# Optimization experiments

Measured on AMD Instinct MI355X. Metric: run time of the kernel, lower is better.

The kernel has to match this reference:

```python
import jax, jax.numpy as jnp
import numpy as np

L, E, D, R, B = 3, 4, 1024, 64, 32768

def setup_inputs() -> dict:
    key = jax.random.key(0)
    ks = jax.random.split(key, 6)
    sU = (2.0 / (D + R)) ** 0.5  # xavier_normal std for [E, D, R]
    sC = (2.0 / (R + R)) ** 0.5
    sG = (2.0 / (D + 1)) ** 0.5
    return {
        "inputs": jax.random.normal(ks[0], (B, D), jnp.float32),
        "U": jax.random.normal(ks[1], (L, E, D, R), jnp.float32) * sU,
        "V": jax.random.normal(ks[2], (L, E, D, R), jnp.float32) * sU,
        "C": jax.random.normal(ks[3], (L, E, R, R), jnp.float32) * sC,
        "gating_w": jax.random.normal(ks[4], (E, D), jnp.float32) * sG,
        "bias": jnp.zeros((L, D), jnp.float32),
    }

def reference(inputs, U, V, C, gating_w, bias):
    x0 = inputs            # [B, D]
    x_l = inputs           # [B, D]
    for i in range(L):
        # per-expert gating scores on current x_l, softmax over experts
        gate = jax.nn.softmax(jnp.einsum("bd,ed->be", x_l, gating_w), axis=1)  # [B, E]
        # low-rank cross: V^T x -> tanh -> C v -> tanh -> U v
        v = jnp.tanh(jnp.einsum("bd,edr->ber", x_l, V[i]))     # [B, E, R]
        v = jnp.tanh(jnp.einsum("ers,bes->ber", C[i], v))      # [B, E, R]
        uv = jnp.einsum("edr,ber->bed", U[i], v)               # [B, E, D]
        dot = x0[:, None, :] * (uv + bias[i][None, None, :])   # [B, E, D]
        moe = jnp.einsum("bed,be->bd", dot, gate)              # [B, D]
        x_l = moe + x_l
    return x_l
```

## Files before the change

kernel.cpp:

```cpp
#include <hip/hip_runtime.h>
#include <hip/hip_bf16.h>

typedef __bf16 bf16_t;
typedef bf16_t bf16x8 __attribute__((ext_vector_type(8)));
typedef float f32x4 __attribute__((ext_vector_type(4)));

#define L_NUM 3
#define E_NUM 4
#define D_DIM 1024
#define R_DIM 64
#define B_ROWS 32768
#define BT 32
#define TPB 512
#define N1 272
#define XL_STRIDE 1032
#define T1_STRIDE 264

#define VT_ELEMS (L_NUM * N1 * D_DIM)
#define UT_ELEMS (L_NUM * D_DIM * 256)
#define CB_ELEMS (L_NUM * E_NUM * R_DIM * R_DIM)

#define MFMA16(a, b, c) __builtin_amdgcn_mfma_f32_16x16x32_bf16((a), (b), (c), 0, 0, 0)

__device__ __forceinline__ ushort f2b(float f) {
  union { float f; unsigned u; } x; x.f = f;
  unsigned r = (x.u + 0x7fffu + ((x.u >> 16) & 1u)) >> 16;
  return (ushort)r;
}
__device__ __forceinline__ float b2f(ushort h) {
  union { unsigned u; float f; } x; x.u = ((unsigned)h) << 16;
  return x.f;
}
__device__ __forceinline__ float tanh_fast(float x) {
  float cx = fminf(fmaxf(x, -15.f), 15.f);
  float e = __expf(2.f * cx);
  return (e - 1.f) / (e + 1.f);
}


__global__ void pack_vt_kernel(const float* __restrict__ V, const float* __restrict__ gw,
                               ushort* __restrict__ vt) {
  int idx = blockIdx.x * 256 + threadIdx.x;
  if (idx >= VT_ELEMS) return;
  int d = idx & (D_DIM - 1);
  int n = (idx >> 10) % N1;
  int l = idx / (N1 * D_DIM);
  float val = 0.f;
  if (n < 256) {
    int e = n >> 6, r = n & 63;
    val = V[(((l * E_NUM + e) * D_DIM) + d) * R_DIM + r];
  } else if (n < 260) {
    val = gw[(n - 256) * D_DIM + d];
  }
  vt[idx] = f2b(val);
}

__global__ void pack_ut_kernel(const float* __restrict__ U, ushort* __restrict__ ut) {
  int idx = blockIdx.x * 256 + threadIdx.x;
  if (idx >= UT_ELEMS) return;
  int er = idx & 255;
  int d = (idx >> 8) & (D_DIM - 1);
  int l = idx >> 18;
  int e = er >> 6, r = er & 63;
  ut[idx] = f2b(U[((l * E_NUM + e) * D_DIM + d) * R_DIM + r]);
}

__global__ void pack_cb_kernel(const float* __restrict__ C, ushort* __restrict__ cb) {
  int idx = blockIdx.x * 256 + threadIdx.x;
  if (idx >= CB_ELEMS) return;
  cb[idx] = f2b(C[idx]);
}


__global__ __launch_bounds__(TPB, 2) void crossnet_fused(
    const float* __restrict__ inputs, const float* __restrict__ bias,
    const ushort* __restrict__ Vt, const ushort* __restrict__ Ut,
    const ushort* __restrict__ Cb, float* __restrict__ out) {
  __shared__ ushort xl[BT * XL_STRIDE];
  __shared__ ushort x0s[BT * XL_STRIDE];
  __shared__ ushort t1[BT * T1_STRIDE];
  __shared__ float glog[BT * 4];
  __shared__ float gate[BT * 4];

  const int tid = threadIdx.x;
  const int wave = tid >> 6;
  const int lane = tid & 63;
  const int l15 = lane & 15;
  const int quad = lane >> 4;
  const long rowbase = (long)blockIdx.x * BT;

  #pragma unroll
  for (int i = 0; i < 16; ++i) {
    int idx = tid + i * TPB;
    int r = idx >> 8;
    int c4 = idx & 255;
    float4 v = ((const float4*)(inputs + (rowbase + r) * D_DIM))[c4];
    ushort4 h;
    h.x = f2b(v.x); h.y = f2b(v.y); h.z = f2b(v.z); h.w = f2b(v.w);
    *(ushort4*)&xl[r * XL_STRIDE + c4 * 4] = h;
    *(ushort4*)&x0s[r * XL_STRIDE + c4 * 4] = h;
  }

  float xlr[8][2][4];
  #pragma unroll
  for (int nt = 0; nt < 8; ++nt)
    #pragma unroll
    for (int m = 0; m < 2; ++m)
      #pragma unroll
      for (int rg = 0; rg < 4; ++rg) {
        int row = m * 16 + quad * 4 + rg;
        int col = wave * 128 + nt * 16 + l15;
        xlr[nt][m][rg] = inputs[(rowbase + row) * D_DIM + col];
      }
  __syncthreads();

  const f32x4 zf = {0.f, 0.f, 0.f, 0.f};

  for (int l = 0; l < L_NUM; ++l) {
    const ushort* vtl = Vt + l * N1 * D_DIM;
    const ushort* utl = Ut + l * D_DIM * 256;
    const ushort* cbl = Cb + l * E_NUM * R_DIM * R_DIM;

    f32x4 acc1[3][2];
    #pragma unroll
    for (int t = 0; t < 3; ++t) { acc1[t][0] = zf; acc1[t][1] = zf; }

    const ushort* xa0 = &xl[l15 * XL_STRIDE + quad * 8];
    const ushort* xa1 = &xl[(16 + l15) * XL_STRIDE + quad * 8];
    const ushort* vb0 = vtl + (wave * 32 + l15) * D_DIM + quad * 8;
    const ushort* vb1 = vb0 + 16 * D_DIM;
    if (wave == 7) {
      const ushort* vb2 = vtl + (256 + l15) * D_DIM + quad * 8;
      #pragma unroll 4
      for (int k0 = 0; k0 < D_DIM; k0 += 32) {
        bf16x8 a0 = *(const bf16x8*)(xa0 + k0);
        bf16x8 a1 = *(const bf16x8*)(xa1 + k0);
        bf16x8 b0 = *(const bf16x8*)(vb0 + k0);
        bf16x8 b1 = *(const bf16x8*)(vb1 + k0);
        bf16x8 b2 = *(const bf16x8*)(vb2 + k0);
        acc1[0][0] = MFMA16(a0, b0, acc1[0][0]);
        acc1[0][1] = MFMA16(a1, b0, acc1[0][1]);
        acc1[1][0] = MFMA16(a0, b1, acc1[1][0]);
        acc1[1][1] = MFMA16(a1, b1, acc1[1][1]);
        acc1[2][0] = MFMA16(a0, b2, acc1[2][0]);
        acc1[2][1] = MFMA16(a1, b2, acc1[2][1]);
      }
    } else {
      #pragma unroll 4
      for (int k0 = 0; k0 < D_DIM; k0 += 32) {
        bf16x8 a0 = *(const bf16x8*)(xa0 + k0);
        bf16x8 a1 = *(const bf16x8*)(xa1 + k0);
        bf16x8 b0 = *(const bf16x8*)(vb0 + k0);
        bf16x8 b1 = *(const bf16x8*)(vb1 + k0);
        acc1[0][0] = MFMA16(a0, b0, acc1[0][0]);
        acc1[0][1] = MFMA16(a1, b0, acc1[0][1]);
        acc1[1][0] = MFMA16(a0, b1, acc1[1][0]);
        acc1[1][1] = MFMA16(a1, b1, acc1[1][1]);
      }
    }

    #pragma unroll
    for (int t = 0; t < 2; ++t) {
      int ncol = wave * 32 + t * 16 + l15;
      #pragma unroll
      for (int m = 0; m < 2; ++m)
        #pragma unroll
        for (int rg = 0; rg < 4; ++rg) {
          int row = m * 16 + quad * 4 + rg;
          t1[row * T1_STRIDE + ncol] = f2b(tanh_fast(acc1[t][m][rg]));
        }
    }
    if (wave == 7 && l15 < 4) {
      #pragma unroll
      for (int m = 0; m < 2; ++m)
        #pragma unroll
        for (int rg = 0; rg < 4; ++rg)
          glog[(m * 16 + quad * 4 + rg) * 4 + l15] = acc1[2][m][rg];
    }
    __syncthreads();

    if (tid < BT) {
      float g0 = glog[tid * 4 + 0], g1 = glog[tid * 4 + 1];
      float g2 = glog[tid * 4 + 2], g3 = glog[tid * 4 + 3];
      float mx = fmaxf(fmaxf(g0, g1), fmaxf(g2, g3));
      float e0 = __expf(g0 - mx), e1 = __expf(g1 - mx);
      float e2 = __expf(g2 - mx), e3 = __expf(g3 - mx);
      float inv = 1.f / (e0 + e1 + e2 + e3);
      gate[tid * 4 + 0] = e0 * inv; gate[tid * 4 + 1] = e1 * inv;
      gate[tid * 4 + 2] = e2 * inv; gate[tid * 4 + 3] = e3 * inv;
    }

    const int e = wave >> 1;
    const int nh = wave & 1;
    f32x4 acc2[2][2];
    acc2[0][0] = zf; acc2[0][1] = zf; acc2[1][0] = zf; acc2[1][1] = zf;
    #pragma unroll
    for (int k0 = 0; k0 < 64; k0 += 32) {
      bf16x8 a0 = *(const bf16x8*)&t1[l15 * T1_STRIDE + e * 64 + k0 + quad * 8];
      bf16x8 a1 = *(const bf16x8*)&t1[(16 + l15) * T1_STRIDE + e * 64 + k0 + quad * 8];
      bf16x8 b0 = *(const bf16x8*)&cbl[(e * 64 + nh * 32 + l15) * 64 + k0 + quad * 8];
      bf16x8 b1 = *(const bf16x8*)&cbl[(e * 64 + nh * 32 + 16 + l15) * 64 + k0 + quad * 8];
      acc2[0][0] = MFMA16(a0, b0, acc2[0][0]);
      acc2[0][1] = MFMA16(a1, b0, acc2[0][1]);
      acc2[1][0] = MFMA16(a0, b1, acc2[1][0]);
      acc2[1][1] = MFMA16(a1, b1, acc2[1][1]);
    }
    __syncthreads();
    #pragma unroll
    for (int t = 0; t < 2; ++t) {
      int ncol = e * 64 + nh * 32 + t * 16 + l15;
      #pragma unroll
      for (int m = 0; m < 2; ++m)
        #pragma unroll
        for (int rg = 0; rg < 4; ++rg) {
          int row = m * 16 + quad * 4 + rg;
          float g = gate[row * 4 + e];
          t1[row * T1_STRIDE + ncol] = f2b(g * tanh_fast(acc2[t][m][rg]));
        }
    }
    __syncthreads();

    f32x4 acc3[8][2];
    #pragma unroll
    for (int nt = 0; nt < 8; ++nt) { acc3[nt][0] = zf; acc3[nt][1] = zf; }
    const ushort* wa0 = &t1[l15 * T1_STRIDE + quad * 8];
    const ushort* wa1 = &t1[(16 + l15) * T1_STRIDE + quad * 8];
    const ushort* ub = utl + (wave * 128 + l15) * 256 + quad * 8;
    #pragma unroll 2
    for (int k0 = 0; k0 < 256; k0 += 32) {
      bf16x8 a0 = *(const bf16x8*)(wa0 + k0);
      bf16x8 a1 = *(const bf16x8*)(wa1 + k0);
      #pragma unroll
      for (int nt = 0; nt < 8; ++nt) {
        bf16x8 b = *(const bf16x8*)(ub + nt * 16 * 256 + k0);
        acc3[nt][0] = MFMA16(a0, b, acc3[nt][0]);
        acc3[nt][1] = MFMA16(a1, b, acc3[nt][1]);
      }
    }

    #pragma unroll
    for (int nt = 0; nt < 8; ++nt) {
      int col = wave * 128 + nt * 16 + l15;
      float bv = bias[l * D_DIM + col];
      #pragma unroll
      for (int m = 0; m < 2; ++m)
        #pragma unroll
        for (int rg = 0; rg < 4; ++rg) {
          int row = m * 16 + quad * 4 + rg;
          float x0v = b2f(x0s[row * XL_STRIDE + col]);
          float xn = xlr[nt][m][rg] + x0v * (acc3[nt][m][rg] + bv);
          xlr[nt][m][rg] = xn;
          xl[row * XL_STRIDE + col] = f2b(xn);
        }
    }
    __syncthreads();
  }

  #pragma unroll
  for (int nt = 0; nt < 8; ++nt) {
    int col = wave * 128 + nt * 16 + l15;
    #pragma unroll
    for (int m = 0; m < 2; ++m)
      #pragma unroll
      for (int rg = 0; rg < 4; ++rg) {
        int row = m * 16 + quad * 4 + rg;
        out[(rowbase + row) * D_DIM + col] = xlr[nt][m][rg];
      }
  }
}

extern "C" void kernel_launch(void* const* d_in, const int* in_sizes, int n_in,
                              void* d_out, int out_size, void* d_ws, size_t ws_size,
                              hipStream_t stream) {
  (void)in_sizes; (void)n_in; (void)out_size; (void)ws_size;
  const float* inputs = (const float*)d_in[0];
  const float* U      = (const float*)d_in[1];
  const float* V      = (const float*)d_in[2];
  const float* C      = (const float*)d_in[3];
  const float* gw     = (const float*)d_in[4];
  const float* bias   = (const float*)d_in[5];
  float* out = (float*)d_out;

  ushort* vt = (ushort*)d_ws;
  ushort* ut = vt + VT_ELEMS;
  ushort* cb = ut + UT_ELEMS;

  pack_vt_kernel<<<(VT_ELEMS + 255) / 256, 256, 0, stream>>>(V, gw, vt);
  pack_ut_kernel<<<(UT_ELEMS + 255) / 256, 256, 0, stream>>>(U, ut);
  pack_cb_kernel<<<(CB_ELEMS + 255) / 256, 256, 0, stream>>>(C, cb);

  crossnet_fused<<<B_ROWS / BT, TPB, 0, stream>>>(inputs, bias, vt, ut, cb, out);
}
```

Before: 685.0 us.

## Shrink LDS and registers with swizzled bf16 residual and in-register x0

Drops the padded fp32 residual held in registers and the separate x0 shared buffer. The residual now lives only as bf16 in an XOR-swizzled shared tile, and x0 is kept as packed bf16 pairs in registers. Gating softmax is computed with wave shuffles and passed through a global workspace. The U projection is split into two halves, the final layer writes the output directly, and launch bounds ask for 4 blocks per CU. The aim is to cut LDS and register use so more blocks fit per CU, and to avoid bank conflicts without padding. The risks are register spills under the tighter bound and extra rounding from carrying the residual in bf16 between layers.

```diff
diff --git a/kernel.cpp b/kernel.cpp
--- a/kernel.cpp
+++ b/kernel.cpp
@@ -8,17 +8,15 @@
 #define L_NUM 3
 #define E_NUM 4
 #define D_DIM 1024
-#define R_DIM 64
 #define B_ROWS 32768
 #define BT 32
 #define TPB 512
 #define N1 272
-#define XL_STRIDE 1032
-#define T1_STRIDE 264
 
 #define VT_ELEMS (L_NUM * N1 * D_DIM)
 #define UT_ELEMS (L_NUM * D_DIM * 256)
-#define CB_ELEMS (L_NUM * E_NUM * R_DIM * R_DIM)
+#define CB_ELEMS (L_NUM * E_NUM * 64 * 64)
+#define GWS_BYTE_OFF ((VT_ELEMS + UT_ELEMS + CB_ELEMS) * 2)
 
 #define MFMA16(a, b, c) __builtin_amdgcn_mfma_f32_16x16x32_bf16((a), (b), (c), 0, 0, 0)
 
@@ -31,10 +29,19 @@
   union { unsigned u; float f; } x; x.u = ((unsigned)h) << 16;
   return x.f;
 }
+__device__ __forceinline__ float u2f_lo(unsigned u) {
+  union { unsigned u; float f; } x; x.u = u << 16; return x.f;
+}
+__device__ __forceinline__ float u2f_hi(unsigned u) {
+  union { unsigned u; float f; } x; x.u = u & 0xffff0000u; return x.f;
+}
 __device__ __forceinline__ float tanh_fast(float x) {
   float cx = fminf(fmaxf(x, -15.f), 15.f);
   float e = __expf(2.f * cx);
   return (e - 1.f) / (e + 1.f);
+}
+__device__ __forceinline__ int swz(int r, int c, int cols) {
+  return r * cols + ((((c >> 3) ^ (r & 7)) << 3) | (c & 7));
 }
 
 
@@ -48,7 +55,7 @@
   float val = 0.f;
   if (n < 256) {
     int e = n >> 6, r = n & 63;
-    val = V[(((l * E_NUM + e) * D_DIM) + d) * R_DIM + r];
+    val = V[(((l * E_NUM + e) * D_DIM) + d) * 64 + r];
   } else if (n < 260) {
     val = gw[(n - 256) * D_DIM + d];
   }
@@ -62,7 +69,7 @@
   int d = (idx >> 8) & (D_DIM - 1);
   int l = idx >> 18;
   int e = er >> 6, r = er & 63;
-  ut[idx] = f2b(U[((l * E_NUM + e) * D_DIM + d) * R_DIM + r]);
+  ut[idx] = f2b(U[((l * E_NUM + e) * D_DIM + d) * 64 + r]);
 }
 
 __global__ void pack_cb_kernel(const float* __restrict__ C, ushort* __restrict__ cb) {
@@ -72,22 +79,22 @@
 }
 
 
-__global__ __launch_bounds__(TPB, 2) void crossnet_fused(
+__global__ __launch_bounds__(TPB, 4) void crossnet_fused(
     const float* __restrict__ inputs, const float* __restrict__ bias,
     const ushort* __restrict__ Vt, const ushort* __restrict__ Ut,
-    const ushort* __restrict__ Cb, float* __restrict__ out) {
-  __shared__ ushort xl[BT * XL_STRIDE];
-  __shared__ ushort x0s[BT * XL_STRIDE];
-  __shared__ ushort t1[BT * T1_STRIDE];
-  __shared__ float glog[BT * 4];
-  __shared__ float gate[BT * 4];
+    const ushort* __restrict__ Cb, float* __restrict__ gws,
+    float* __restrict__ out) {
+  __shared__ ushort xl[BT * 1024];
+  __shared__ ushort t1s[BT * 256];
 
   const int tid = threadIdx.x;
   const int wave = tid >> 6;
   const int lane = tid & 63;
   const int l15 = lane & 15;
   const int quad = lane >> 4;
+  const int r7 = l15 & 7;
   const long rowbase = (long)blockIdx.x * BT;
+  float* gwb = gws + (long)blockIdx.x * (BT * E_NUM);
 
   #pragma unroll
   for (int i = 0; i < 16; ++i) {
@@ -97,47 +104,50 @@
     float4 v = ((const float4*)(inputs + (rowbase + r) * D_DIM))[c4];
     ushort4 h;
     h.x = f2b(v.x); h.y = f2b(v.y); h.z = f2b(v.z); h.w = f2b(v.w);
-    *(ushort4*)&xl[r * XL_STRIDE + c4 * 4] = h;
-    *(ushort4*)&x0s[r * XL_STRIDE + c4 * 4] = h;
+    int off = r * 1024 + ((((c4 >> 1) ^ (r & 7)) << 3) | ((c4 & 1) << 2));
+    *(ushort4*)&xl[off] = h;
   }
-
-  float xlr[8][2][4];
+  __syncthreads();
+
+  unsigned x0p[8][2][2];
   #pragma unroll
-  for (int nt = 0; nt < 8; ++nt)
+  for (int c8 = 0; c8 < 8; ++c8) {
+    int col = wave * 128 + c8 * 16 + l15;
     #pragma unroll
     for (int m = 0; m < 2; ++m)
       #pragma unroll
-      for (int rg = 0; rg < 4; ++rg) {
-        int row = m * 16 + quad * 4 + rg;
-        int col = wave * 128 + nt * 16 + l15;
-        xlr[nt][m][rg] = inputs[(rowbase + row) * D_DIM + col];
-      }
-  __syncthreads();
+      for (int pr = 0; pr < 2; ++pr) {
+        int r0 = m * 16 + quad * 4 + 2 * pr;
+        unsigned lo = xl[swz(r0, col, 1024)];
+        unsigned hi = xl[swz(r0 + 1, col, 1024)];
+        x0p[c8][m][pr] = lo | (hi << 16);
+      }
+  }
 
   const f32x4 zf = {0.f, 0.f, 0.f, 0.f};
 
   for (int l = 0; l < L_NUM; ++l) {
     const ushort* vtl = Vt + l * N1 * D_DIM;
     const ushort* utl = Ut + l * D_DIM * 256;
-    const ushort* cbl = Cb + l * E_NUM * R_DIM * R_DIM;
+    const ushort* cbl = Cb + l * E_NUM * 64 * 64;
 
     f32x4 acc1[3][2];
     #pragma unroll
     for (int t = 0; t < 3; ++t) { acc1[t][0] = zf; acc1[t][1] = zf; }
 
-    const ushort* xa0 = &xl[l15 * XL_STRIDE + quad * 8];
-    const ushort* xa1 = &xl[(16 + l15) * XL_STRIDE + quad * 8];
     const ushort* vb0 = vtl + (wave * 32 + l15) * D_DIM + quad * 8;
     const ushort* vb1 = vb0 + 16 * D_DIM;
+    const int abase = l15 * 1024;
     if (wave == 7) {
       const ushort* vb2 = vtl + (256 + l15) * D_DIM + quad * 8;
       #pragma unroll 4
-      for (int k0 = 0; k0 < D_DIM; k0 += 32) {
-        bf16x8 a0 = *(const bf16x8*)(xa0 + k0);
-        bf16x8 a1 = *(const bf16x8*)(xa1 + k0);
-        bf16x8 b0 = *(const bf16x8*)(vb0 + k0);
-        bf16x8 b1 = *(const bf16x8*)(vb1 + k0);
-        bf16x8 b2 = *(const bf16x8*)(vb2 + k0);
+      for (int t = 0; t < 32; ++t) {
+        int ch = ((4 * t + quad) ^ r7) << 3;
+        bf16x8 a0 = *(const bf16x8*)&xl[abase + ch];
+        bf16x8 a1 = *(const bf16x8*)&xl[abase + ch + 16 * 1024];
+        bf16x8 b0 = *(const bf16x8*)(vb0 + t * 32);
+        bf16x8 b1 = *(const bf16x8*)(vb1 + t * 32);
+        bf16x8 b2 = *(const bf16x8*)(vb2 + t * 32);
         acc1[0][0] = MFMA16(a0, b0, acc1[0][0]);
         acc1[0][1] = MFMA16(a1, b0, acc1[0][1]);
         acc1[1][0] = MFMA16(a0, b1, acc1[1][0]);
@@ -147,11 +157,12 @@
       }
     } else {
       #pragma unroll 4
-      for (int k0 = 0; k0 < D_DIM; k0 += 32) {
-        bf16x8 a0 = *(const bf16x8*)(xa0 + k0);
-        bf16x8 a1 = *(const bf16x8*)(xa1 + k0);
-        bf16x8 b0 = *(const bf16x8*)(vb0 + k0);
-        bf16x8 b1 = *(const bf16x8*)(vb1 + k0);
+      for (int t = 0; t < 32; ++t) {
+        int ch = ((4 * t + quad) ^ r7) << 3;
+        bf16x8 a0 = *(const bf16x8*)&xl[abase + ch];
+        bf16x8 a1 = *(const bf16x8*)&xl[abase + ch + 16 * 1024];
+        bf16x8 b0 = *(const bf16x8*)(vb0 + t * 32);
+        bf16x8 b1 = *(const bf16x8*)(vb1 + t * 32);
         acc1[0][0] = MFMA16(a0, b0, acc1[0][0]);
         acc1[0][1] = MFMA16(a1, b0, acc1[0][1]);
         acc1[1][0] = MFMA16(a0, b1, acc1[1][0]);
@@ -160,112 +171,118 @@
     }
 
     #pragma unroll
-    for (int t = 0; t < 2; ++t) {
-      int ncol = wave * 32 + t * 16 + l15;
+    for (int tt = 0; tt < 2; ++tt) {
+      int ncol = wave * 32 + tt * 16 + l15;
       #pragma unroll
       for (int m = 0; m < 2; ++m)
         #pragma unroll
         for (int rg = 0; rg < 4; ++rg) {
           int row = m * 16 + quad * 4 + rg;
-          t1[row * T1_STRIDE + ncol] = f2b(tanh_fast(acc1[t][m][rg]));
+          t1s[swz(row, ncol, 256)] = f2b(tanh_fast(acc1[tt][m][rg]));
         }
     }
-    if (wave == 7 && l15 < 4) {
+    if (wave == 7) {
       #pragma unroll
       for (int m = 0; m < 2; ++m)
         #pragma unroll
-        for (int rg = 0; rg < 4; ++rg)
-          glog[(m * 16 + quad * 4 + rg) * 4 + l15] = acc1[2][m][rg];
+        for (int rg = 0; rg < 4; ++rg) {
+          float g = acc1[2][m][rg];
+          float mx = fmaxf(g, __shfl_xor(g, 1));
+          mx = fmaxf(mx, __shfl_xor(mx, 2));
+          float ex = __expf(g - mx);
+          float s = ex + __shfl_xor(ex, 1);
+          s = s + __shfl_xor(s, 2);
+          if (l15 < 4) {
+            int row = m * 16 + quad * 4 + rg;
+            gwb[row * 4 + l15] = ex / s;
+          }
+        }
     }
     __syncthreads();
-
-    if (tid < BT) {
-      float g0 = glog[tid * 4 + 0], g1 = glog[tid * 4 + 1];
-      float g2 = glog[tid * 4 + 2], g3 = glog[tid * 4 + 3];
-      float mx = fmaxf(fmaxf(g0, g1), fmaxf(g2, g3));
-      float e0 = __expf(g0 - mx), e1 = __expf(g1 - mx);
-      float e2 = __expf(g2 - mx), e3 = __expf(g3 - mx);
-      float inv = 1.f / (e0 + e1 + e2 + e3);
-      gate[tid * 4 + 0] = e0 * inv; gate[tid * 4 + 1] = e1 * inv;
-      gate[tid * 4 + 2] = e2 * inv; gate[tid * 4 + 3] = e3 * inv;
-    }
 
     const int e = wave >> 1;
     const int nh = wave & 1;
     f32x4 acc2[2][2];
     acc2[0][0] = zf; acc2[0][1] = zf; acc2[1][0] = zf; acc2[1][1] = zf;
-    #pragma unroll
-    for (int k0 = 0; k0 < 64; k0 += 32) {
-      bf16x8 a0 = *(const bf16x8*)&t1[l15 * T1_STRIDE + e * 64 + k0 + quad * 8];
-      bf16x8 a1 = *(const bf16x8*)&t1[(16 + l15) * T1_STRIDE + e * 64 + k0 + quad * 8];
-      bf16x8 b0 = *(const bf16x8*)&cbl[(e * 64 + nh * 32 + l15) * 64 + k0 + quad * 8];
-      bf16x8 b1 = *(const bf16x8*)&cbl[(e * 64 + nh * 32 + 16 + l15) * 64 + k0 + quad * 8];
-      acc2[0][0] = MFMA16(a0, b0, acc2[0][0]);
-      acc2[0][1] = MFMA16(a1, b0, acc2[0][1]);
-      acc2[1][0] = MFMA16(a0, b1, acc2[1][0]);
-      acc2[1][1] = MFMA16(a1, b1, acc2[1][1]);
-    }
+    {
+      const ushort* cb0 = cbl + (e * 64 + nh * 32 + l15) * 64 + quad * 8;
+      const ushort* cb1 = cb0 + 16 * 64;
+      #pragma unroll
+      for (int t = 0; t < 2; ++t) {
+        int ch = ((8 * e + 4 * t + quad) ^ r7) << 3;
+        bf16x8 a0 = *(const bf16x8*)&t1s[l15 * 256 + ch];
+        bf16x8 a1 = *(const bf16x8*)&t1s[l15 * 256 + ch + 16 * 256];
+        bf16x8 b0 = *(const bf16x8*)(cb0 + t * 32);
+        bf16x8 b1 = *(const bf16x8*)(cb1 + t * 32);
+        acc2[0][0] = MFMA16(a0, b0, acc2[0][0]);
+        acc2[0][1] = MFMA16(a1, b0, acc2[0][1]);
+        acc2[1][0] = MFMA16(a0, b1, acc2[1][0]);
+        acc2[1][1] = MFMA16(a1, b1, acc2[1][1]);
+      }
+    }
+    float g8[2][4];
+    #pragma unroll
+    for (int m = 0; m < 2; ++m)
+      #pragma unroll
+      for (int rg = 0; rg < 4; ++rg)
+        g8[m][rg] = gwb[(m * 16 + quad * 4 + rg) * 4 + e];
     __syncthreads();
     #pragma unroll
-    for (int t = 0; t < 2; ++t) {
-      int ncol = e * 64 + nh * 32 + t * 16 + l15;
+    for (int tt = 0; tt < 2; ++tt) {
+      int ncol = e * 64 + nh * 32 + tt * 16 + l15;
       #pragma unroll
       for (int m = 0; m < 2; ++m)
         #pragma unroll
         for (int rg = 0; rg < 4; ++rg) {
           int row = m * 16 + quad * 4 + rg;
-          float g = gate[row * 4 + e];
-          t1[row * T1_STRIDE + ncol] = f2b(g * tanh_fast(acc2[t][m][rg]));
+          t1s[swz(row, ncol, 256)] = f2b(g8[m][rg] * tanh_fast(acc2[tt][m][rg]));
         }
     }
     __syncthreads();
 
-    f32x4 acc3[8][2];
-    #pragma unroll
-    for (int nt = 0; nt < 8; ++nt) { acc3[nt][0] = zf; acc3[nt][1] = zf; }
-    const ushort* wa0 = &t1[l15 * T1_STRIDE + quad * 8];
-    const ushort* wa1 = &t1[(16 + l15) * T1_STRIDE + quad * 8];
-    const ushort* ub = utl + (wave * 128 + l15) * 256 + quad * 8;
-    #pragma unroll 2
-    for (int k0 = 0; k0 < 256; k0 += 32) {
-      bf16x8 a0 = *(const bf16x8*)(wa0 + k0);
-      bf16x8 a1 = *(const bf16x8*)(wa1 + k0);
-      #pragma unroll
-      for (int nt = 0; nt < 8; ++nt) {
-        bf16x8 b = *(const bf16x8*)(ub + nt * 16 * 256 + k0);
-        acc3[nt][0] = MFMA16(a0, b, acc3[nt][0]);
-        acc3[nt][1] = MFMA16(a1, b, acc3[nt][1]);
-      }
-    }
-
-    #pragma unroll
-    for (int nt = 0; nt < 8; ++nt) {
-      int col = wave * 128 + nt * 16 + l15;
-      float bv = bias[l * D_DIM + col];
-      #pragma unroll
-      for (int m = 0; m < 2; ++m)
-        #pragma unroll
-        for (int rg = 0; rg < 4; ++rg) {
-          int row = m * 16 + quad * 4 + rg;
-          float x0v = b2f(x0s[row * XL_STRIDE + col]);
-          float xn = xlr[nt][m][rg] + x0v * (acc3[nt][m][rg] + bv);
-          xlr[nt][m][rg] = xn;
-          xl[row * XL_STRIDE + col] = f2b(xn);
+    #pragma unroll
+    for (int half = 0; half < 2; ++half) {
+      f32x4 acc3[4][2];
+      #pragma unroll
+      for (int nt = 0; nt < 4; ++nt) { acc3[nt][0] = zf; acc3[nt][1] = zf; }
+      const ushort* ub = utl + (wave * 128 + half * 64 + l15) * 256 + quad * 8;
+      #pragma unroll
+      for (int t = 0; t < 8; ++t) {
+        int ch = ((4 * t + quad) ^ r7) << 3;
+        bf16x8 a0 = *(const bf16x8*)&t1s[l15 * 256 + ch];
+        bf16x8 a1 = *(const bf16x8*)&t1s[l15 * 256 + ch + 16 * 256];
+        #pragma unroll
+        for (int nt = 0; nt < 4; ++nt) {
+          bf16x8 b = *(const bf16x8*)(ub + nt * 16 * 256 + t * 32);
+          acc3[nt][0] = MFMA16(a0, b, acc3[nt][0]);
+          acc3[nt][1] = MFMA16(a1, b, acc3[nt][1]);
         }
+      }
+      #pragma unroll
+      for (int nt = 0; nt < 4; ++nt) {
+        int c8 = half * 4 + nt;
+        int col = wave * 128 + c8 * 16 + l15;
+        float bv = bias[l * D_DIM + col];
+        #pragma unroll
+        for (int m = 0; m < 2; ++m)
+          #pragma unroll
+          for (int pr = 0; pr < 2; ++pr) {
+            unsigned u = x0p[c8][m][pr];
+            float x0e = u2f_lo(u), x0o = u2f_hi(u);
+            int r0 = m * 16 + quad * 4 + 2 * pr;
+            float xe = b2f(xl[swz(r0, col, 1024)]) + x0e * (acc3[nt][m][2 * pr] + bv);
+            float xo = b2f(xl[swz(r0 + 1, col, 1024)]) + x0o * (acc3[nt][m][2 * pr + 1] + bv);
+            if (l < 2) {
+              xl[swz(r0, col, 1024)] = f2b(xe);
+              xl[swz(r0 + 1, col, 1024)] = f2b(xo);
+            } else {
+              out[(rowbase + r0) * D_DIM + col] = xe;
+              out[(rowbase + r0 + 1) * D_DIM + col] = xo;
+            }
+          }
+      }
     }
     __syncthreads();
-  }
-
-  #pragma unroll
-  for (int nt = 0; nt < 8; ++nt) {
-    int col = wave * 128 + nt * 16 + l15;
-    #pragma unroll
-    for (int m = 0; m < 2; ++m)
-      #pragma unroll
-      for (int rg = 0; rg < 4; ++rg) {
-        int row = m * 16 + quad * 4 + rg;
-        out[(rowbase + row) * D_DIM + col] = xlr[nt][m][rg];
-      }
   }
 }
 
@@ -284,10 +301,11 @@
   ushort* vt = (ushort*)d_ws;
   ushort* ut = vt + VT_ELEMS;
   ushort* cb = ut + UT_ELEMS;
+  float* gws = (float*)((char*)d_ws + GWS_BYTE_OFF);
 
   pack_vt_kernel<<<(VT_ELEMS + 255) / 256, 256, 0, stream>>>(V, gw, vt);
   pack_ut_kernel<<<(UT_ELEMS + 255) / 256, 256, 0, stream>>>(U, ut);
   pack_cb_kernel<<<(CB_ELEMS + 255) / 256, 256, 0, stream>>>(C, cb);
 
-  crossnet_fused<<<B_ROWS / BT, TPB, 0, stream>>>(inputs, bias, vt, ut, cb, out);
-}
+  crossnet_fused<<<B_ROWS / BT, TPB, 0, stream>>>(inputs, bias, vt, ut, cb, gws, out);
+}
```

Result: slower. 1.181 ms (+72.3%).
